# Optimization experiments

Measured on AMD Instinct MI355X. Metric: run time of the kernel, lower is better.

Reference implementation:

```python
import jax, jax.numpy as jnp
import numpy as np

N, NFEAT, NHID, E, P, STEPS = 100000, 256, 128, 3200000, 200000, 5
EPS = 1e-6


def _p(key, shape, scale=0.05):
    return (jax.random.normal(key, shape, dtype=jnp.float32) * scale)


def setup_inputs() -> dict:
    key = jax.random.key(0)
    ks = jax.random.split(key, 32)
    inp = {
        "inputs": jax.random.normal(ks[0], (N, NFEAT), dtype=jnp.float32),
        "edge_row": jnp.sort(jax.random.randint(ks[1], (E,), 0, N, dtype=jnp.int32)),
        "edge_col": jax.random.randint(ks[2], (E,), 0, N, dtype=jnp.int32),
        "edge_w": jax.random.uniform(ks[3], (E,), dtype=jnp.float32),
        "x_idx": jax.random.randint(ks[4], (P,), 0, N, dtype=jnp.int32),
        "y_idx": jax.random.randint(ks[5], (P,), 0, N, dtype=jnp.int32),
        # input gates: Linear(nfeat, nhid) with bias
        "Wr_in": _p(ks[6], (NFEAT, NHID)), "br_in": _p(ks[7], (NHID,)),
        "Wi_in": _p(ks[8], (NFEAT, NHID)), "bi_in": _p(ks[9], (NHID,)),
        "Wn_in": _p(ks[10], (NFEAT, NHID)), "bn_in": _p(ks[11], (NHID,)),
        # hidden GCN gates: weight_self + weight_neighbor, no bias
        "Hr_self": _p(ks[12], (NHID, NHID)), "Hr_nb": _p(ks[13], (NHID, NHID)),
        "Hi_self": _p(ks[14], (NHID, NHID)), "Hi_nb": _p(ks[15], (NHID, NHID)),
        "Hh_self": _p(ks[16], (NHID, NHID)), "Hh_nb": _p(ks[17], (NHID, NHID)),
        # post-GRU MLP fc1..fc3
        "W1": _p(ks[18], (NHID, NHID)), "b1": _p(ks[19], (NHID,)),
        "W2": _p(ks[20], (NHID, NHID)), "b2": _p(ks[21], (NHID,)),
        "W3": _p(ks[22], (NHID, NHID)), "b3": _p(ks[23], (NHID,)),
        # layernorm
        "gamma": jnp.ones((NHID,), jnp.float32), "beta": jnp.zeros((NHID,), jnp.float32),
        # decoder
        "Wd1": _p(ks[24], (2 * NHID, NHID)), "bd1": _p(ks[25], (NHID,)),
        "Wd2": _p(ks[26], (NHID, 1)), "bd2": _p(ks[27], (1,)),
    }
    return inp


def _spmm(row, col, w, x):
    # sparse [N,N] @ dense [N,D] via gather + segment_sum
    return jax.ops.segment_sum(x[col] * w[:, None], row, num_segments=N)


def _gcn(h, w_self, w_nb, row, col, ew):
    return h @ w_self + _spmm(row, col, ew, h @ w_nb)


def reference(inputs, edge_row, edge_col, edge_w, x_idx, y_idx,
              Wr_in, br_in, Wi_in, bi_in, Wn_in, bn_in,
              Hr_self, Hr_nb, Hi_self, Hi_nb, Hh_self, Hh_nb,
              W1, b1, W2, b2, W3, b3, gamma, beta,
              Wd1, bd1, Wd2, bd2):
    # input-gate projections are loop-invariant
    in_r = inputs @ Wr_in + br_in
    in_i = inputs @ Wi_in + bi_in
    in_n = inputs @ Wn_in + bn_in
    h = jnp.zeros((inputs.shape[0], NHID), dtype=inputs.dtype)
    for _ in range(STEPS):
        r = jax.nn.sigmoid(in_r + _gcn(h, Hr_self, Hr_nb, edge_row, edge_col, edge_w))
        i = jax.nn.sigmoid(in_i + _gcn(h, Hi_self, Hi_nb, edge_row, edge_col, edge_w))
        n = jnp.tanh(in_n + r * _gcn(h, Hh_self, Hh_nb, edge_row, edge_col, edge_w))
        h = (1.0 - i) * n + i * h
    x = jax.nn.relu(h @ W1 + b1)
    x = jax.nn.relu(x @ W2 + b2)
    x = jax.nn.relu(x @ W3 + b3)
    # torch LayerNorm variant: unbiased std, eps added to std (not var)
    mean = jnp.mean(x, axis=-1, keepdims=True)
    std = jnp.std(x, axis=-1, keepdims=True, ddof=1)
    z = gamma * (x - mean) / (std + EPS) + beta
    # MLP decoder on node pairs
    hcat = jnp.concatenate([z[x_idx], z[y_idx]], axis=1)  # [P, 2*nhid]
    d = jax.nn.relu(hcat @ Wd1 + bd1)
    d = jax.nn.sigmoid(d @ Wd2 + bd2)  # [P, 1]
    return d, z
```

## Files before the change

### kernel.cpp

```cpp
#include <hip/hip_runtime.h>
#include <hip/hip_bf16.h>

#define N_NODES 100000
#define NFEAT 256
#define NHID 128
#define NEDGE 3200000
#define NPAIR 200000
#define NSTEPS 5

typedef __attribute__((ext_vector_type(8))) short short8x;
typedef __attribute__((ext_vector_type(4))) float f32x4;

__device__ __forceinline__ float sigmoidf_(float x) {
    return 1.f / (1.f + __expf(-x));
}
__device__ __forceinline__ unsigned short f2bf_bits(float f) {
    union { float f; unsigned int u; } c; c.f = f;
    unsigned int r = (c.u + 0x7FFFu + ((c.u >> 16) & 1u)) >> 16;
    return (unsigned short)r;
}
__device__ __forceinline__ float bf_bits2f(unsigned short b) {
    union { float f; unsigned int u; } c; c.u = ((unsigned int)b) << 16;
    return c.f;
}
__device__ __forceinline__ int swz8(int row, int q) {
    return row * 32 + ((q + (row >> 1)) & 3) * 8;
}

__global__ void zero_u16(unsigned short* __restrict__ p, long long n) {
    long long i = (long long)blockIdx.x * blockDim.x + threadIdx.x;
    if (i < n) p[i] = 0;
}

__global__ void build_row_ptr(const int* __restrict__ rows, int E, int N, int* __restrict__ row_ptr) {
    int i = blockIdx.x * blockDim.x + threadIdx.x;
    if (i > N) return;
    int lo = 0, hi = E;
    while (lo < hi) {
        int mid = (lo + hi) >> 1;
        if (rows[mid] < i) lo = mid + 1; else hi = mid;
    }
    row_ptr[i] = lo;
}

__global__ void pack_kmajor(const float* __restrict__ W, int K, int NCsrc,
                            unsigned short* __restrict__ out, int NCtot, int coff, int koff) {
    int idx = blockIdx.x * blockDim.x + threadIdx.x;
    if (idx >= K * NCsrc) return;
    int k = idx / NCsrc, j = idx - k * NCsrc;
    int kg = k + koff;
    out[(size_t)(kg >> 5) * NCtot * 32 + (size_t)(coff + j) * 32 + (kg & 31)] = f2bf_bits(W[idx]);
}

__global__ void pack_bin(const float* __restrict__ br, const float* __restrict__ bi,
                         const float* __restrict__ bn, float* __restrict__ bin) {
    int i = blockIdx.x * blockDim.x + threadIdx.x;
    if (i >= 384) return;
    bin[i] = (i < 128) ? br[i] : (i < 256) ? bi[i - 128] : bn[i - 256];
}

__global__ __launch_bounds__(256) void spmm_bf16_ilp(
    const int* __restrict__ row_ptr, const int* __restrict__ col,
    const float* __restrict__ w, const unsigned short* __restrict__ hbf,
    unsigned short* __restrict__ hsbf, int N)
{
    int v = blockIdx.x * 4 + (threadIdx.x >> 6);
    int lane = threadIdx.x & 63;
    int g = lane >> 4;
    int l16 = lane & 15;
    if (v >= N) return;
    int e0 = row_ptr[v], e1 = row_ptr[v + 1];
    float acc[8] = {};
    int e = e0 + g;
    for (; e + 4 < e1; e += 8) {
        int c1 = col[e], c2 = col[e + 4];
        float w1 = w[e], w2 = w[e + 4];
        const uint4 h1 = *reinterpret_cast<const uint4*>(hbf + (size_t)c1 * NHID + l16 * 8);
        const uint4 h2 = *reinterpret_cast<const uint4*>(hbf + (size_t)c2 * NHID + l16 * 8);
        acc[0] += w1 * bf_bits2f((unsigned short)h1.x) + w2 * bf_bits2f((unsigned short)h2.x);
        acc[1] += w1 * bf_bits2f((unsigned short)(h1.x >> 16)) + w2 * bf_bits2f((unsigned short)(h2.x >> 16));
        acc[2] += w1 * bf_bits2f((unsigned short)h1.y) + w2 * bf_bits2f((unsigned short)h2.y);
        acc[3] += w1 * bf_bits2f((unsigned short)(h1.y >> 16)) + w2 * bf_bits2f((unsigned short)(h2.y >> 16));
        acc[4] += w1 * bf_bits2f((unsigned short)h1.z) + w2 * bf_bits2f((unsigned short)h2.z);
        acc[5] += w1 * bf_bits2f((unsigned short)(h1.z >> 16)) + w2 * bf_bits2f((unsigned short)(h2.z >> 16));
        acc[6] += w1 * bf_bits2f((unsigned short)h1.w) + w2 * bf_bits2f((unsigned short)h2.w);
        acc[7] += w1 * bf_bits2f((unsigned short)(h1.w >> 16)) + w2 * bf_bits2f((unsigned short)(h2.w >> 16));
    }
    for (; e < e1; e += 4) {
        int cc = col[e];
        float we = w[e];
        const uint4 hv = *reinterpret_cast<const uint4*>(hbf + (size_t)cc * NHID + l16 * 8);
        acc[0] += we * bf_bits2f((unsigned short)hv.x);
        acc[1] += we * bf_bits2f((unsigned short)(hv.x >> 16));
        acc[2] += we * bf_bits2f((unsigned short)hv.y);
        acc[3] += we * bf_bits2f((unsigned short)(hv.y >> 16));
        acc[4] += we * bf_bits2f((unsigned short)hv.z);
        acc[5] += we * bf_bits2f((unsigned short)(hv.z >> 16));
        acc[6] += we * bf_bits2f((unsigned short)hv.w);
        acc[7] += we * bf_bits2f((unsigned short)(hv.w >> 16));
    }
    #pragma unroll
    for (int q = 0; q < 8; q++) {
        acc[q] += __shfl_xor(acc[q], 16, 64);
        acc[q] += __shfl_xor(acc[q], 32, 64);
    }
    if (g == 0) {
        uint4 o;
        o.x = (unsigned int)f2bf_bits(acc[0]) | ((unsigned int)f2bf_bits(acc[1]) << 16);
        o.y = (unsigned int)f2bf_bits(acc[2]) | ((unsigned int)f2bf_bits(acc[3]) << 16);
        o.z = (unsigned int)f2bf_bits(acc[4]) | ((unsigned int)f2bf_bits(acc[5]) << 16);
        o.w = (unsigned int)f2bf_bits(acc[6]) | ((unsigned int)f2bf_bits(acc[7]) << 16);
        *reinterpret_cast<uint4*>(hsbf + (size_t)v * NHID + l16 * 8) = o;
    }
}

__global__ __launch_bounds__(256, 2) void gate_step_mfma(
    const unsigned short* __restrict__ hsbf, unsigned short* __restrict__ hbf,
    const unsigned short* __restrict__ IN, const unsigned short* __restrict__ WBg, int M)
{
    __shared__ unsigned short As[64 * 32];
    __shared__ unsigned short Bs[384 * 32];

    const int tid = threadIdx.x;
    const int wid = tid >> 6;
    const int lane = tid & 63;
    const int row0 = blockIdx.x * 64;
    const int l15 = lane & 15;
    const int lhi = lane >> 4;

    f32x4 acc[3][2][4] = {};

    const int ar = tid >> 2;
    const int aq = tid & 3;
    const int agr = row0 + ar;

    for (int s = 0; s < 8; s++) {
        {
            short8x va = short8x(0);
            if (agr < M) {
                const unsigned short* src = (s < 4)
                    ? (hbf  + (size_t)agr * 128 + s * 32)
                    : (hsbf + (size_t)agr * 128 + (s - 4) * 32);
                va = *reinterpret_cast<const short8x*>(src + aq * 8);
            }
            *reinterpret_cast<short8x*>(&As[swz8(ar, aq)]) = va;
        }
        {
            const unsigned short* wbs = WBg + (size_t)s * 384 * 32;
            #pragma unroll
            for (int i = 0; i < 6; i++) {
                int id = tid + i * 256;
                int c = id >> 2, q = id & 3;
                short8x vb = *reinterpret_cast<const short8x*>(wbs + id * 8);
                *reinterpret_cast<short8x*>(&Bs[swz8(c, q)]) = vb;
            }
        }
        __syncthreads();

        short8x a[4];
        #pragma unroll
        for (int rb = 0; rb < 4; rb++)
            a[rb] = *reinterpret_cast<const short8x*>(&As[swz8(16 * rb + l15, lhi)]);
        #pragma unroll
        for (int p = 0; p < 3; p++) {
            #pragma unroll
            for (int cb = 0; cb < 2; cb++) {
                int c0 = 128 * p + 32 * wid + 16 * cb + l15;
                short8x b = *reinterpret_cast<const short8x*>(&Bs[swz8(c0, lhi)]);
                #pragma unroll
                for (int rb = 0; rb < 4; rb++)
                    acc[p][cb][rb] = __builtin_amdgcn_mfma_f32_16x16x32_bf16(b, a[rb], acc[p][cb][rb], 0, 0, 0);
            }
        }
        __syncthreads();
    }

    #pragma unroll
    for (int rb = 0; rb < 4; rb++) {
        int row = row0 + 16 * rb + l15;
        if (row >= M) continue;
        size_t ib = (size_t)row * 384;
        size_t ob = (size_t)row * 128;
        #pragma unroll
        for (int cb = 0; cb < 2; cb++) {
            int cq = 32 * wid + 16 * cb + 4 * lhi;
            const ushort4 vr = *reinterpret_cast<const ushort4*>(IN + ib + cq);
            const ushort4 vi = *reinterpret_cast<const ushort4*>(IN + ib + 128 + cq);
            const ushort4 vn = *reinterpret_cast<const ushort4*>(IN + ib + 256 + cq);
            const ushort4 vh = *reinterpret_cast<const ushort4*>(hbf + ob + cq);
            const unsigned short ra[4] = {vr.x, vr.y, vr.z, vr.w};
            const unsigned short ia[4] = {vi.x, vi.y, vi.z, vi.w};
            const unsigned short na[4] = {vn.x, vn.y, vn.z, vn.w};
            const unsigned short ha[4] = {vh.x, vh.y, vh.z, vh.w};
            unsigned short oa[4];
            #pragma unroll
            for (int j = 0; j < 4; j++) {
                float g_r = acc[0][cb][rb][j] + bf_bits2f(ra[j]);
                float g_i = acc[1][cb][rb][j] + bf_bits2f(ia[j]);
                float rr = sigmoidf_(g_r);
                float gi = sigmoidf_(g_i);
                float nn = tanhf(bf_bits2f(na[j]) + rr * acc[2][cb][rb][j]);
                oa[j] = f2bf_bits((1.f - gi) * nn + gi * bf_bits2f(ha[j]));
            }
            ushort4 st; st.x = oa[0]; st.y = oa[1]; st.z = oa[2]; st.w = oa[3];
            *reinterpret_cast<ushort4*>(hbf + ob + cq) = st;
        }
    }
}

template<int K, int NC, bool F32IN, bool RELU, bool BF16OUT>
__global__ __launch_bounds__(256, 2) void mfma_gemm(
    const void* __restrict__ Xv, const unsigned short* __restrict__ WBx,
    const float* __restrict__ bias, void* __restrict__ C, int M)
{
    constexpr int KS = K / 32;
    constexpr int BI = NC / 64;
    constexpr int NCW = NC / 4;
    constexpr int CB = NCW / 16;
    __shared__ unsigned short As[64 * 32];
    __shared__ unsigned short Bs[NC * 32];

    const int tid = threadIdx.x;
    const int wid = tid >> 6;
    const int lane = tid & 63;
    const int l15 = lane & 15;
    const int lhi = lane >> 4;
    const int row0 = blockIdx.x * 64;

    f32x4 acc[CB][4] = {};

    const int ar = tid >> 2;
    const int aq = tid & 3;
    const int agr = row0 + ar;

    for (int s = 0; s < KS; s++) {
        {
            short8x va = short8x(0);
            if (agr < M) {
                if (F32IN) {
                    const float* src = (const float*)Xv + (size_t)agr * K + s * 32 + aq * 8;
                    const float4 f0 = *reinterpret_cast<const float4*>(src);
                    const float4 f1 = *reinterpret_cast<const float4*>(src + 4);
                    va[0] = (short)f2bf_bits(f0.x); va[1] = (short)f2bf_bits(f0.y);
                    va[2] = (short)f2bf_bits(f0.z); va[3] = (short)f2bf_bits(f0.w);
                    va[4] = (short)f2bf_bits(f1.x); va[5] = (short)f2bf_bits(f1.y);
                    va[6] = (short)f2bf_bits(f1.z); va[7] = (short)f2bf_bits(f1.w);
                } else {
                    va = *reinterpret_cast<const short8x*>(
                        (const unsigned short*)Xv + (size_t)agr * K + s * 32 + aq * 8);
                }
            }
            *reinterpret_cast<short8x*>(&As[swz8(ar, aq)]) = va;
        }
        {
            const unsigned short* wbs = WBx + (size_t)s * NC * 32;
            #pragma unroll
            for (int i = 0; i < BI; i++) {
                int id = tid + i * 256;
                int c = id >> 2, q = id & 3;
                short8x vb = *reinterpret_cast<const short8x*>(wbs + id * 8);
                *reinterpret_cast<short8x*>(&Bs[swz8(c, q)]) = vb;
            }
        }
        __syncthreads();

        short8x a[4];
        #pragma unroll
        for (int rb = 0; rb < 4; rb++)
            a[rb] = *reinterpret_cast<const short8x*>(&As[swz8(16 * rb + l15, lhi)]);
        #pragma unroll
        for (int cb = 0; cb < CB; cb++) {
            int c0 = NCW * wid + 16 * cb + l15;
            short8x b = *reinterpret_cast<const short8x*>(&Bs[swz8(c0, lhi)]);
            #pragma unroll
            for (int rb = 0; rb < 4; rb++)
                acc[cb][rb] = __builtin_amdgcn_mfma_f32_16x16x32_bf16(b, a[rb], acc[cb][rb], 0, 0, 0);
        }
        __syncthreads();
    }

    #pragma unroll
    for (int rb = 0; rb < 4; rb++) {
        int row = row0 + 16 * rb + l15;
        if (row >= M) continue;
        #pragma unroll
        for (int cb = 0; cb < CB; cb++) {
            int cq = NCW * wid + 16 * cb + 4 * lhi;
            float4 bv = make_float4(0.f, 0.f, 0.f, 0.f);
            if (bias) bv = *reinterpret_cast<const float4*>(bias + cq);
            const float bva[4] = {bv.x, bv.y, bv.z, bv.w};
            float o[4];
            #pragma unroll
            for (int j = 0; j < 4; j++) {
                float v = acc[cb][rb][j] + bva[j];
                if (RELU) v = fmaxf(v, 0.f);
                o[j] = v;
            }
            if (BF16OUT) {
                ushort4 st;
                st.x = f2bf_bits(o[0]); st.y = f2bf_bits(o[1]);
                st.z = f2bf_bits(o[2]); st.w = f2bf_bits(o[3]);
                *reinterpret_cast<ushort4*>((unsigned short*)C + (size_t)row * NC + cq) = st;
            } else {
                float4 st; st.x = o[0]; st.y = o[1]; st.z = o[2]; st.w = o[3];
                *reinterpret_cast<float4*>((float*)C + (size_t)row * NC + cq) = st;
            }
        }
    }
}

__global__ __launch_bounds__(256) void layernorm_bf(
    const unsigned short* __restrict__ x, const float* __restrict__ gamma,
    const float* __restrict__ beta, float* __restrict__ zout,
    unsigned short* __restrict__ zbf, int N)
{
    int v = blockIdx.x * 4 + (threadIdx.x >> 6);
    int lane = threadIdx.x & 63;
    if (v >= N) return;
    const unsigned short* xr = x + (size_t)v * NHID;
    float x0 = bf_bits2f(xr[lane]), x1 = bf_bits2f(xr[lane + 64]);
    float s = x0 + x1;
    #pragma unroll
    for (int off = 32; off; off >>= 1) s += __shfl_xor(s, off, 64);
    float mean = s * (1.f / 128.f);
    float d0 = x0 - mean, d1 = x1 - mean;
    float vs = d0 * d0 + d1 * d1;
    #pragma unroll
    for (int off = 32; off; off >>= 1) vs += __shfl_xor(vs, off, 64);
    float std_ = sqrtf(vs / 127.f);
    float inv = 1.f / (std_ + 1e-6f);
    float z0 = gamma[lane] * d0 * inv + beta[lane];
    float z1 = gamma[lane + 64] * d1 * inv + beta[lane + 64];
    size_t o = (size_t)v * NHID;
    zout[o + lane] = z0;
    zout[o + lane + 64] = z1;
    zbf[o + lane] = f2bf_bits(z0);
    zbf[o + lane + 64] = f2bf_bits(z1);
}

__global__ __launch_bounds__(256) void decoder_pairs(
    const unsigned short* __restrict__ UV,
    const int* __restrict__ xi, const int* __restrict__ yi,
    const float* __restrict__ bd1, const float* __restrict__ Wd2,
    const float* __restrict__ bd2, float* __restrict__ dout, int P)
{
    __shared__ float b1s[128], w2s[128];
    if (threadIdx.x < 128) {
        b1s[threadIdx.x] = bd1[threadIdx.x];
        w2s[threadIdx.x] = Wd2[threadIdx.x];
    }
    __syncthreads();
    int p = blockIdx.x * 256 + threadIdx.x;
    if (p >= P) return;
    const unsigned short* ur = UV + (size_t)xi[p] * 256;
    const unsigned short* vr = UV + (size_t)yi[p] * 256 + 128;
    float part = 0.f;
    #pragma unroll
    for (int j0 = 0; j0 < 128; j0 += 8) {
        const uint4 ua = *reinterpret_cast<const uint4*>(ur + j0);
        const uint4 va = *reinterpret_cast<const uint4*>(vr + j0);
        float uf[8], vf[8];
        uf[0] = bf_bits2f((unsigned short)ua.x); uf[1] = bf_bits2f((unsigned short)(ua.x >> 16));
        uf[2] = bf_bits2f((unsigned short)ua.y); uf[3] = bf_bits2f((unsigned short)(ua.y >> 16));
        uf[4] = bf_bits2f((unsigned short)ua.z); uf[5] = bf_bits2f((unsigned short)(ua.z >> 16));
        uf[6] = bf_bits2f((unsigned short)ua.w); uf[7] = bf_bits2f((unsigned short)(ua.w >> 16));
        vf[0] = bf_bits2f((unsigned short)va.x); vf[1] = bf_bits2f((unsigned short)(va.x >> 16));
        vf[2] = bf_bits2f((unsigned short)va.y); vf[3] = bf_bits2f((unsigned short)(va.y >> 16));
        vf[4] = bf_bits2f((unsigned short)va.z); vf[5] = bf_bits2f((unsigned short)(va.z >> 16));
        vf[6] = bf_bits2f((unsigned short)va.w); vf[7] = bf_bits2f((unsigned short)(va.w >> 16));
        #pragma unroll
        for (int q = 0; q < 8; q++) {
            float t = uf[q] + vf[q] + b1s[j0 + q];
            part += fmaxf(t, 0.f) * w2s[j0 + q];
        }
    }
    dout[p] = sigmoidf_(part + bd2[0]);
}

extern "C" void kernel_launch(void* const* d_in, const int* in_sizes, int n_in,
                              void* d_out, int out_size, void* d_ws, size_t ws_size,
                              hipStream_t stream) {
    const float* inputs = (const float*)d_in[0];
    const int* edge_row = (const int*)d_in[1];
    const int* edge_col = (const int*)d_in[2];
    const float* edge_w = (const float*)d_in[3];
    const int* x_idx = (const int*)d_in[4];
    const int* y_idx = (const int*)d_in[5];
    const float* Wr_in = (const float*)d_in[6];  const float* br_in = (const float*)d_in[7];
    const float* Wi_in = (const float*)d_in[8];  const float* bi_in = (const float*)d_in[9];
    const float* Wn_in = (const float*)d_in[10]; const float* bn_in = (const float*)d_in[11];
    const float* Hr_self = (const float*)d_in[12]; const float* Hr_nb = (const float*)d_in[13];
    const float* Hi_self = (const float*)d_in[14]; const float* Hi_nb = (const float*)d_in[15];
    const float* Hh_self = (const float*)d_in[16]; const float* Hh_nb = (const float*)d_in[17];
    const float* W1 = (const float*)d_in[18]; const float* b1 = (const float*)d_in[19];
    const float* W2 = (const float*)d_in[20]; const float* b2 = (const float*)d_in[21];
    const float* W3 = (const float*)d_in[22]; const float* b3 = (const float*)d_in[23];
    const float* gamma = (const float*)d_in[24]; const float* beta = (const float*)d_in[25];
    const float* Wd1 = (const float*)d_in[26]; const float* bd1 = (const float*)d_in[27];
    const float* Wd2 = (const float*)d_in[28]; const float* bd2 = (const float*)d_in[29];

    float* out_d = (float*)d_out;
    float* out_z = ((float*)d_out) + NPAIR;

    char* base = (char*)d_ws;
    size_t off = 0;
    auto take = [&](size_t bytes) { void* p = base + off; off = (off + bytes + 255) & ~(size_t)255; return p; };
    int*            row_ptr = (int*)           take((size_t)(N_NODES + 1) * 4);
    unsigned short* WBg     = (unsigned short*)take((size_t)8 * 384 * 32 * 2);
    unsigned short* WBin    = (unsigned short*)take((size_t)8 * 384 * 32 * 2);
    unsigned short* WB1     = (unsigned short*)take((size_t)4 * 128 * 32 * 2);
    unsigned short* WB2     = (unsigned short*)take((size_t)4 * 128 * 32 * 2);
    unsigned short* WB3     = (unsigned short*)take((size_t)4 * 128 * 32 * 2);
    unsigned short* WBd     = (unsigned short*)take((size_t)4 * 256 * 32 * 2);
    float*          bin     = (float*)         take(384 * 4);
    unsigned short* IN      = (unsigned short*)take((size_t)N_NODES * 384 * 2);
    unsigned short* hbf     = (unsigned short*)take((size_t)N_NODES * NHID * 2);
    unsigned short* hsbf    = (unsigned short*)take((size_t)N_NODES * NHID * 2);
    if (off > ws_size) return;

    build_row_ptr<<<(N_NODES + 256) / 256, 256, 0, stream>>>(edge_row, NEDGE, N_NODES, row_ptr);
    pack_kmajor<<<64, 256, 0, stream>>>(Hr_self, 128, 128, WBg, 384, 0, 0);
    pack_kmajor<<<64, 256, 0, stream>>>(Hi_self, 128, 128, WBg, 384, 128, 0);
    pack_kmajor<<<64, 256, 0, stream>>>(Hh_self, 128, 128, WBg, 384, 256, 0);
    pack_kmajor<<<64, 256, 0, stream>>>(Hr_nb,   128, 128, WBg, 384, 0, 128);
    pack_kmajor<<<64, 256, 0, stream>>>(Hi_nb,   128, 128, WBg, 384, 128, 128);
    pack_kmajor<<<64, 256, 0, stream>>>(Hh_nb,   128, 128, WBg, 384, 256, 128);
    pack_kmajor<<<128, 256, 0, stream>>>(Wr_in, 256, 128, WBin, 384, 0, 0);
    pack_kmajor<<<128, 256, 0, stream>>>(Wi_in, 256, 128, WBin, 384, 128, 0);
    pack_kmajor<<<128, 256, 0, stream>>>(Wn_in, 256, 128, WBin, 384, 256, 0);
    pack_kmajor<<<64, 256, 0, stream>>>(W1, 128, 128, WB1, 128, 0, 0);
    pack_kmajor<<<64, 256, 0, stream>>>(W2, 128, 128, WB2, 128, 0, 0);
    pack_kmajor<<<64, 256, 0, stream>>>(W3, 128, 128, WB3, 128, 0, 0);
    pack_kmajor<<<64, 256, 0, stream>>>(Wd1,             128, 128, WBd, 256, 0, 0);
    pack_kmajor<<<64, 256, 0, stream>>>(Wd1 + 128 * 128, 128, 128, WBd, 256, 128, 0);
    pack_bin<<<2, 256, 0, stream>>>(br_in, bi_in, bn_in, bin);
    {
        long long n = (long long)N_NODES * NHID;
        zero_u16<<<(unsigned)((n + 255) / 256), 256, 0, stream>>>(hbf, n);
    }
    int grid64 = (N_NODES + 63) / 64;
    mfma_gemm<256, 384, true, false, true><<<grid64, 256, 0, stream>>>(inputs, WBin, bin, IN, N_NODES);
    for (int s = 0; s < NSTEPS; s++) {
        spmm_bf16_ilp<<<(N_NODES + 3) / 4, 256, 0, stream>>>(row_ptr, edge_col, edge_w, hbf, hsbf, N_NODES);
        gate_step_mfma<<<grid64, 256, 0, stream>>>(hsbf, hbf, IN, WBg, N_NODES);
    }
    unsigned short* x1 = hsbf;
    unsigned short* x2 = IN;
    unsigned short* x3 = hbf;
    mfma_gemm<128, 128, false, true, true><<<grid64, 256, 0, stream>>>(hbf, WB1, b1, x1, N_NODES);
    mfma_gemm<128, 128, false, true, true><<<grid64, 256, 0, stream>>>(x1, WB2, b2, x2, N_NODES);
    mfma_gemm<128, 128, false, true, true><<<grid64, 256, 0, stream>>>(x2, WB3, b3, x3, N_NODES);
    unsigned short* zbf = hsbf;
    layernorm_bf<<<(N_NODES + 3) / 4, 256, 0, stream>>>(x3, gamma, beta, out_z, zbf, N_NODES);
    unsigned short* UV = IN;
    mfma_gemm<128, 256, false, false, true><<<grid64, 256, 0, stream>>>(zbf, WBd, nullptr, UV, N_NODES);
    decoder_pairs<<<(NPAIR + 255) / 256, 256, 0, stream>>>(
        UV, x_idx, y_idx, bd1, Wd2, bd2, out_d, NPAIR);
}
```

Baseline: 1.131 ms.

## Fuse MLP, LayerNorm and decoder projection into one tile kernel; unroll SpMM

Replaces three MLP GEMM launches, the LayerNorm kernel and the decoder projection GEMM with a single kernel. Each 64-row tile stays in shared memory through all layers, LayerNorm and the UV projection, so the intermediate activations no longer round-trip through global memory. It also widens the SpMM edge loop from 2 to 4 independent gathers per iteration to get more loads in flight. The cost is larger shared memory and register use per block, and less parallelism per layer inside the fused kernel.

```diff
diff --git a/kernel.cpp b/kernel.cpp
--- a/kernel.cpp
+++ b/kernel.cpp
@@ -58,6 +58,16 @@
     if (i >= 384) return;
     bin[i] = (i < 128) ? br[i] : (i < 256) ? bi[i - 128] : bn[i - 256];
 }
+
+#define SPMM_ACC(hv, we) { \
+    acc[0] += (we) * bf_bits2f((unsigned short)(hv).x); \
+    acc[1] += (we) * bf_bits2f((unsigned short)((hv).x >> 16)); \
+    acc[2] += (we) * bf_bits2f((unsigned short)(hv).y); \
+    acc[3] += (we) * bf_bits2f((unsigned short)((hv).y >> 16)); \
+    acc[4] += (we) * bf_bits2f((unsigned short)(hv).z); \
+    acc[5] += (we) * bf_bits2f((unsigned short)((hv).z >> 16)); \
+    acc[6] += (we) * bf_bits2f((unsigned short)(hv).w); \
+    acc[7] += (we) * bf_bits2f((unsigned short)((hv).w >> 16)); }
 
 __global__ __launch_bounds__(256) void spmm_bf16_ilp(
     const int* __restrict__ row_ptr, const int* __restrict__ col,
@@ -72,32 +82,20 @@
     int e0 = row_ptr[v], e1 = row_ptr[v + 1];
     float acc[8] = {};
     int e = e0 + g;
-    for (; e + 4 < e1; e += 8) {
-        int c1 = col[e], c2 = col[e + 4];
-        float w1 = w[e], w2 = w[e + 4];
+    for (; e + 12 < e1; e += 16) {
+        int c1 = col[e], c2 = col[e + 4], c3 = col[e + 8], c4 = col[e + 12];
+        float w1 = w[e], w2 = w[e + 4], w3 = w[e + 8], w4 = w[e + 12];
         const uint4 h1 = *reinterpret_cast<const uint4*>(hbf + (size_t)c1 * NHID + l16 * 8);
         const uint4 h2 = *reinterpret_cast<const uint4*>(hbf + (size_t)c2 * NHID + l16 * 8);
-        acc[0] += w1 * bf_bits2f((unsigned short)h1.x) + w2 * bf_bits2f((unsigned short)h2.x);
-        acc[1] += w1 * bf_bits2f((unsigned short)(h1.x >> 16)) + w2 * bf_bits2f((unsigned short)(h2.x >> 16));
-        acc[2] += w1 * bf_bits2f((unsigned short)h1.y) + w2 * bf_bits2f((unsigned short)h2.y);
-        acc[3] += w1 * bf_bits2f((unsigned short)(h1.y >> 16)) + w2 * bf_bits2f((unsigned short)(h2.y >> 16));
-        acc[4] += w1 * bf_bits2f((unsigned short)h1.z) + w2 * bf_bits2f((unsigned short)h2.z);
-        acc[5] += w1 * bf_bits2f((unsigned short)(h1.z >> 16)) + w2 * bf_bits2f((unsigned short)(h2.z >> 16));
-        acc[6] += w1 * bf_bits2f((unsigned short)h1.w) + w2 * bf_bits2f((unsigned short)h2.w);
-        acc[7] += w1 * bf_bits2f((unsigned short)(h1.w >> 16)) + w2 * bf_bits2f((unsigned short)(h2.w >> 16));
+        const uint4 h3 = *reinterpret_cast<const uint4*>(hbf + (size_t)c3 * NHID + l16 * 8);
+        const uint4 h4 = *reinterpret_cast<const uint4*>(hbf + (size_t)c4 * NHID + l16 * 8);
+        SPMM_ACC(h1, w1) SPMM_ACC(h2, w2) SPMM_ACC(h3, w3) SPMM_ACC(h4, w4)
     }
     for (; e < e1; e += 4) {
         int cc = col[e];
         float we = w[e];
         const uint4 hv = *reinterpret_cast<const uint4*>(hbf + (size_t)cc * NHID + l16 * 8);
-        acc[0] += we * bf_bits2f((unsigned short)hv.x);
-        acc[1] += we * bf_bits2f((unsigned short)(hv.x >> 16));
-        acc[2] += we * bf_bits2f((unsigned short)hv.y);
-        acc[3] += we * bf_bits2f((unsigned short)(hv.y >> 16));
-        acc[4] += we * bf_bits2f((unsigned short)hv.z);
-        acc[5] += we * bf_bits2f((unsigned short)(hv.z >> 16));
-        acc[6] += we * bf_bits2f((unsigned short)hv.w);
-        acc[7] += we * bf_bits2f((unsigned short)(hv.w >> 16));
+        SPMM_ACC(hv, we)
     }
     #pragma unroll
     for (int q = 0; q < 8; q++) {
@@ -309,33 +307,188 @@
     }
 }
 
-__global__ __launch_bounds__(256) void layernorm_bf(
-    const unsigned short* __restrict__ x, const float* __restrict__ gamma,
-    const float* __restrict__ beta, float* __restrict__ zout,
-    unsigned short* __restrict__ zbf, int N)
+#define XT_STRIDE 136
+__global__ __launch_bounds__(256, 2) void mlp_tail(
+    const unsigned short* __restrict__ hbf,
+    const unsigned short* __restrict__ WB1, const unsigned short* __restrict__ WB2,
+    const unsigned short* __restrict__ WB3, const unsigned short* __restrict__ WBd,
+    const float* __restrict__ b1, const float* __restrict__ b2, const float* __restrict__ b3,
+    const float* __restrict__ gamma, const float* __restrict__ beta,
+    float* __restrict__ out_z, unsigned short* __restrict__ UV, int M)
 {
-    int v = blockIdx.x * 4 + (threadIdx.x >> 6);
-    int lane = threadIdx.x & 63;
-    if (v >= N) return;
-    const unsigned short* xr = x + (size_t)v * NHID;
-    float x0 = bf_bits2f(xr[lane]), x1 = bf_bits2f(xr[lane + 64]);
-    float s = x0 + x1;
+    __shared__ unsigned short As[64 * 32];
+    __shared__ unsigned short Bs[256 * 32];
+    __shared__ unsigned short xT[64 * XT_STRIDE];
+
+    const int tid = threadIdx.x;
+    const int wid = tid >> 6;
+    const int lane = tid & 63;
+    const int l15 = lane & 15;
+    const int lhi = lane >> 4;
+    const int row0 = blockIdx.x * 64;
+    const int ar = tid >> 2;
+    const int aq = tid & 3;
+
     #pragma unroll
-    for (int off = 32; off; off >>= 1) s += __shfl_xor(s, off, 64);
-    float mean = s * (1.f / 128.f);
-    float d0 = x0 - mean, d1 = x1 - mean;
-    float vs = d0 * d0 + d1 * d1;
-    #pragma unroll
-    for (int off = 32; off; off >>= 1) vs += __shfl_xor(vs, off, 64);
-    float std_ = sqrtf(vs / 127.f);
-    float inv = 1.f / (std_ + 1e-6f);
-    float z0 = gamma[lane] * d0 * inv + beta[lane];
-    float z1 = gamma[lane + 64] * d1 * inv + beta[lane + 64];
-    size_t o = (size_t)v * NHID;
-    zout[o + lane] = z0;
-    zout[o + lane + 64] = z1;
-    zbf[o + lane] = f2bf_bits(z0);
-    zbf[o + lane + 64] = f2bf_bits(z1);
+    for (int i = 0; i < 4; i++) {
+        int id = tid + i * 256;
+        int r = id >> 4, ch = id & 15;
+        short8x v = short8x(0);
+        if (row0 + r < M)
+            v = *reinterpret_cast<const short8x*>(hbf + (size_t)(row0 + r) * 128 + ch * 8);
+        *reinterpret_cast<short8x*>(&xT[r * XT_STRIDE + ch * 8]) = v;
+    }
+    __syncthreads();
+
+    const unsigned short* WLs[3] = {WB1, WB2, WB3};
+    const float* bLs[3] = {b1, b2, b3};
+    for (int L = 0; L < 3; L++) {
+        f32x4 acc[2][4] = {};
+        for (int s = 0; s < 4; s++) {
+            {
+                short8x va = *reinterpret_cast<const short8x*>(&xT[ar * XT_STRIDE + s * 32 + aq * 8]);
+                *reinterpret_cast<short8x*>(&As[swz8(ar, aq)]) = va;
+            }
+            {
+                const unsigned short* wbs = WLs[L] + (size_t)s * 128 * 32;
+                #pragma unroll
+                for (int i = 0; i < 2; i++) {
+                    int id = tid + i * 256;
+                    int c = id >> 2, q = id & 3;
+                    short8x vb = *reinterpret_cast<const short8x*>(wbs + id * 8);
+                    *reinterpret_cast<short8x*>(&Bs[swz8(c, q)]) = vb;
+                }
+            }
+            __syncthreads();
+            short8x a[4];
+            #pragma unroll
+            for (int rb = 0; rb < 4; rb++)
+                a[rb] = *reinterpret_cast<const short8x*>(&As[swz8(16 * rb + l15, lhi)]);
+            #pragma unroll
+            for (int cb = 0; cb < 2; cb++) {
+                int c0 = 32 * wid + 16 * cb + l15;
+                short8x b = *reinterpret_cast<const short8x*>(&Bs[swz8(c0, lhi)]);
+                #pragma unroll
+                for (int rb = 0; rb < 4; rb++)
+                    acc[cb][rb] = __builtin_amdgcn_mfma_f32_16x16x32_bf16(b, a[rb], acc[cb][rb], 0, 0, 0);
+            }
+            __syncthreads();
+        }
+        #pragma unroll
+        for (int rb = 0; rb < 4; rb++) {
+            int r = 16 * rb + l15;
+            #pragma unroll
+            for (int cb = 0; cb < 2; cb++) {
+                int cq = 32 * wid + 16 * cb + 4 * lhi;
+                const float4 bv = *reinterpret_cast<const float4*>(bLs[L] + cq);
+                const float bva[4] = {bv.x, bv.y, bv.z, bv.w};
+                ushort4 st;
+                unsigned short* o = (unsigned short*)&st;
+                #pragma unroll
+                for (int j = 0; j < 4; j++)
+                    o[j] = f2bf_bits(fmaxf(acc[cb][rb][j] + bva[j], 0.f));
+                *reinterpret_cast<ushort4*>(&xT[r * XT_STRIDE + cq]) = st;
+            }
+        }
+        __syncthreads();
+    }
+
+    {
+        int r = tid >> 2;
+        int grp = tid & 3;
+        int c0 = grp * 32;
+        float xv[32];
+        #pragma unroll
+        for (int k = 0; k < 4; k++) {
+            short8x v = *reinterpret_cast<const short8x*>(&xT[r * XT_STRIDE + c0 + k * 8]);
+            #pragma unroll
+            for (int j = 0; j < 8; j++) xv[k * 8 + j] = bf_bits2f((unsigned short)v[j]);
+        }
+        float s = 0.f;
+        #pragma unroll
+        for (int q = 0; q < 32; q++) s += xv[q];
+        s += __shfl_xor(s, 1, 64);
+        s += __shfl_xor(s, 2, 64);
+        float mean = s * (1.f / 128.f);
+        float vs = 0.f;
+        #pragma unroll
+        for (int q = 0; q < 32; q++) { float d = xv[q] - mean; vs += d * d; }
+        vs += __shfl_xor(vs, 1, 64);
+        vs += __shfl_xor(vs, 2, 64);
+        float inv = 1.f / (sqrtf(vs / 127.f) + 1e-6f);
+        int grow = row0 + r;
+        #pragma unroll
+        for (int k = 0; k < 4; k++) {
+            const float4 gm = *reinterpret_cast<const float4*>(gamma + c0 + k * 8);
+            const float4 gm2 = *reinterpret_cast<const float4*>(gamma + c0 + k * 8 + 4);
+            const float4 bt = *reinterpret_cast<const float4*>(beta + c0 + k * 8);
+            const float4 bt2 = *reinterpret_cast<const float4*>(beta + c0 + k * 8 + 4);
+            const float gms[8] = {gm.x, gm.y, gm.z, gm.w, gm2.x, gm2.y, gm2.z, gm2.w};
+            const float bts[8] = {bt.x, bt.y, bt.z, bt.w, bt2.x, bt2.y, bt2.z, bt2.w};
+            float z[8];
+            short8x zb;
+            #pragma unroll
+            for (int j = 0; j < 8; j++) {
+                z[j] = gms[j] * (xv[k * 8 + j] - mean) * inv + bts[j];
+                zb[j] = (short)f2bf_bits(z[j]);
+            }
+            *reinterpret_cast<short8x*>(&xT[r * XT_STRIDE + c0 + k * 8]) = zb;
+            if (grow < M) {
+                float4 z0 = make_float4(z[0], z[1], z[2], z[3]);
+                float4 z1 = make_float4(z[4], z[5], z[6], z[7]);
+                *reinterpret_cast<float4*>(out_z + (size_t)grow * 128 + c0 + k * 8) = z0;
+                *reinterpret_cast<float4*>(out_z + (size_t)grow * 128 + c0 + k * 8 + 4) = z1;
+            }
+        }
+    }
+    __syncthreads();
+
+    {
+        f32x4 acc[4][4] = {};
+        for (int s = 0; s < 4; s++) {
+            {
+                short8x va = *reinterpret_cast<const short8x*>(&xT[ar * XT_STRIDE + s * 32 + aq * 8]);
+                *reinterpret_cast<short8x*>(&As[swz8(ar, aq)]) = va;
+            }
+            {
+                const unsigned short* wbs = WBd + (size_t)s * 256 * 32;
+                #pragma unroll
+                for (int i = 0; i < 4; i++) {
+                    int id = tid + i * 256;
+                    int c = id >> 2, q = id & 3;
+                    short8x vb = *reinterpret_cast<const short8x*>(wbs + id * 8);
+                    *reinterpret_cast<short8x*>(&Bs[swz8(c, q)]) = vb;
+                }
+            }
+            __syncthreads();
+            short8x a[4];
+            #pragma unroll
+            for (int rb = 0; rb < 4; rb++)
+                a[rb] = *reinterpret_cast<const short8x*>(&As[swz8(16 * rb + l15, lhi)]);
+            #pragma unroll
+            for (int cb = 0; cb < 4; cb++) {
+                int c0 = 64 * wid + 16 * cb + l15;
+                short8x b = *reinterpret_cast<const short8x*>(&Bs[swz8(c0, lhi)]);
+                #pragma unroll
+                for (int rb = 0; rb < 4; rb++)
+                    acc[cb][rb] = __builtin_amdgcn_mfma_f32_16x16x32_bf16(b, a[rb], acc[cb][rb], 0, 0, 0);
+            }
+            __syncthreads();
+        }
+        #pragma unroll
+        for (int rb = 0; rb < 4; rb++) {
+            int row = row0 + 16 * rb + l15;
+            if (row >= M) continue;
+            #pragma unroll
+            for (int cb = 0; cb < 4; cb++) {
+                int cq = 64 * wid + 16 * cb + 4 * lhi;
+                ushort4 st;
+                st.x = f2bf_bits(acc[cb][rb][0]); st.y = f2bf_bits(acc[cb][rb][1]);
+                st.z = f2bf_bits(acc[cb][rb][2]); st.w = f2bf_bits(acc[cb][rb][3]);
+                *reinterpret_cast<ushort4*>(UV + (size_t)row * 256 + cq) = st;
+            }
+        }
+    }
 }
 
 __global__ __launch_bounds__(256) void decoder_pairs(
@@ -444,16 +597,9 @@
         spmm_bf16_ilp<<<(N_NODES + 3) / 4, 256, 0, stream>>>(row_ptr, edge_col, edge_w, hbf, hsbf, N_NODES);
         gate_step_mfma<<<grid64, 256, 0, stream>>>(hsbf, hbf, IN, WBg, N_NODES);
     }
-    unsigned short* x1 = hsbf;
-    unsigned short* x2 = IN;
-    unsigned short* x3 = hbf;
-    mfma_gemm<128, 128, false, true, true><<<grid64, 256, 0, stream>>>(hbf, WB1, b1, x1, N_NODES);
-    mfma_gemm<128, 128, false, true, true><<<grid64, 256, 0, stream>>>(x1, WB2, b2, x2, N_NODES);
-    mfma_gemm<128, 128, false, true, true><<<grid64, 256, 0, stream>>>(x2, WB3, b3, x3, N_NODES);
-    unsigned short* zbf = hsbf;
-    layernorm_bf<<<(N_NODES + 3) / 4, 256, 0, stream>>>(x3, gamma, beta, out_z, zbf, N_NODES);
     unsigned short* UV = IN;
-    mfma_gemm<128, 256, false, false, true><<<grid64, 256, 0, stream>>>(zbf, WBd, nullptr, UV, N_NODES);
+    mlp_tail<<<grid64, 256, 0, stream>>>(hbf, WB1, WB2, WB3, WBd, b1, b2, b3,
+                                         gamma, beta, out_z, UV, N_NODES);
     decoder_pairs<<<(NPAIR + 255) / 256, 256, 0, stream>>>(
         UV, x_idx, y_idx, bd1, Wd2, bd2, out_d, NPAIR);
 }
```

Result: faster. 1.085 ms (-4.0%).
